# Kernel tuning notes

Measured on AMD Instinct MI355X. Metric: run time of the kernel, lower is better.

## Reference

```python
import jax, jax.numpy as jnp
import numpy as np


def setup_inputs() -> dict:
    key = jax.random.key(0)
    k1, k2, k3 = jax.random.split(key, 3)
    B, C, H, W = 8, 256, 64, 64
    l = jax.random.normal(k1, (B, C, H, W), dtype=jnp.float32)
    # 1x1 conv weights [out=C//2, in=C]; scale 1/sqrt(C) so projected features have ~unit variance
    scale = 1.0 / np.sqrt(C)
    w_theta = jax.random.normal(k2, (C // 2, C), dtype=jnp.float32) * scale
    w_phi = jax.random.normal(k3, (C // 2, C), dtype=jnp.float32) * scale
    return {"l": l, "w_theta": w_theta, "w_phi": w_phi}


def reference(l, w_theta, w_phi):
    # NonLocalOp forward with embed=True, softmax=True
    B, C, H, W = l.shape
    E = w_theta.shape[0]  # C // 2
    HW = H * W
    # 1x1 convs == per-pixel linear maps
    theta = jnp.einsum('bchw,ec->behw', l, w_theta).reshape(B, E, HW)  # [B,E,HW]
    phi = jnp.einsum('bchw,ec->behw', l, w_phi).reshape(B, E, HW)      # [B,E,HW]
    g = l.reshape(B, C, HW)                                            # [B,C,HW]
    # scores: theta^T phi over embed channels, scaled by sqrt(C//2)
    scale = 1.0 / jnp.sqrt(jnp.asarray(C // 2, dtype=l.dtype))
    f = jnp.einsum('beq,bek->bqk', theta, phi) * scale                 # [B,HW,HW]
    f = jax.nn.softmax(f, axis=-1)
    out = jnp.einsum('bqk,bck->bcq', f, g).reshape(B, C, H, W)
    return out
```

## Files before the change

### kernel.cpp

```cpp
#include <hip/hip_runtime.h>
#include <stdint.h>

#define NB 8
#define NC 256
#define NE 128
#define NHW 4096

typedef __bf16 v8bf __attribute__((ext_vector_type(8)));
typedef float v4f __attribute__((ext_vector_type(4)));
typedef float v16f __attribute__((ext_vector_type(16)));

#if __has_builtin(__builtin_amdgcn_exp2f)
#define EXP2F(x) __builtin_amdgcn_exp2f(x)
#else
#define EXP2F(x) exp2f(x)
#endif

__device__ __forceinline__ unsigned short f2bf(float x) {
    union { float f; unsigned int u; } v; v.f = x;
    unsigned int r = v.u + 0x7fffu + ((v.u >> 16) & 1u);
    return (unsigned short)(r >> 16);
}

__global__ __launch_bounds__(256) void cast_w_kernel(const float* __restrict__ wt,
                                                     const float* __restrict__ wp,
                                                     unsigned short* __restrict__ Wbf) {
    int i = blockIdx.x * 256 + threadIdx.x;
    const float QS = 0.08838834764831845f * 1.4426950408889634f;
    float v = (i < 32768) ? wt[i] * QS : wp[i - 32768];
    Wbf[i] = f2bf(v);
}

__global__ __launch_bounds__(256, 2) void proj_kernel(const float* __restrict__ l,
                                                      const unsigned short* __restrict__ Wbf,
                                                      unsigned short* __restrict__ Qbf,
                                                      unsigned short* __restrict__ Kbf,
                                                      unsigned short* __restrict__ Vbf) {
    __shared__ __align__(16) unsigned short A[64][264];
    const int tid = threadIdx.x;
    const int b = blockIdx.x & 7;
    const int qt = (blockIdx.x >> 3) << 6;
    const float* lb = l + ((size_t)b * NC * NHW + qt);

    for (int s = 0; s < 16; ++s) {
        int f = tid + s * 256;
        int c = f >> 4, j = f & 15;
        float4 v = *(const float4*)(lb + (size_t)c * NHW + j * 4);
        ushort4 o4;
        o4.x = f2bf(v.x); o4.y = f2bf(v.y); o4.z = f2bf(v.z); o4.w = f2bf(v.w);
        A[j * 4 + 0][c] = o4.x;
        A[j * 4 + 1][c] = o4.y;
        A[j * 4 + 2][c] = o4.z;
        A[j * 4 + 3][c] = o4.w;
        *(ushort4*)(Vbf + (size_t)b * NC * NHW + (size_t)c * NHW + qt + j * 4) = o4;
    }
    __syncthreads();

    const int w = tid >> 6, L = tid & 63;
    const int l15 = L & 15, q4 = L >> 4;
    const v4f vz = {0.f, 0.f, 0.f, 0.f};
    v4f acc[4][4];
    for (int mt = 0; mt < 4; ++mt)
        for (int nt = 0; nt < 4; ++nt) acc[mt][nt] = vz;

    for (int kf = 0; kf < 8; ++kf) {
        int kc = kf * 32 + q4 * 8;
        v8bf a[4], bb[4];
        for (int mt = 0; mt < 4; ++mt)
            a[mt] = *(const v8bf*)&A[mt * 16 + l15][kc];
        for (int nt = 0; nt < 4; ++nt)
            bb[nt] = *(const v8bf*)(Wbf + (w * 64 + nt * 16 + l15) * 256 + kc);
        for (int mt = 0; mt < 4; ++mt)
            for (int nt = 0; nt < 4; ++nt)
                acc[mt][nt] = __builtin_amdgcn_mfma_f32_16x16x32_bf16(a[mt], bb[nt], acc[mt][nt], 0, 0, 0);
    }

    unsigned short* dst = (w < 2) ? Qbf : Kbf;
    const int ebase = (w & 1) * 64;
    for (int mt = 0; mt < 4; ++mt)
        for (int nt = 0; nt < 4; ++nt)
            for (int r = 0; r < 4; ++r) {
                int q = qt + mt * 16 + q4 * 4 + r;
                int e = ebase + nt * 16 + l15;
                dst[((size_t)b * NHW + q) * NE + e] = f2bf(acc[mt][nt][r]);
            }
}

__global__ __launch_bounds__(256, 2) void attn_kernel(const unsigned short* __restrict__ Qbf,
                                                      const unsigned short* __restrict__ Kbf,
                                                      const unsigned short* __restrict__ Vbf,
                                                      float* __restrict__ out) {
    __shared__ __align__(16) unsigned char smem[57344];
    unsigned short* Ku = (unsigned short*)smem;
    unsigned short* Vu = (unsigned short*)(smem + 16384);
    unsigned short* Pu = (unsigned short*)(smem + 49152);
    float* red = (float*)(smem + 49152);

    const int tid = threadIdx.x;
    const int b = blockIdx.x & 7;
    const int qt64 = (blockIdx.x >> 3) << 6;
    const int w = tid >> 6;
    const int L = tid & 63;
    const int l31 = L & 31, hi = L >> 5;
    const int qh = w >> 1, kh = w & 1;
    const int qhp = w & 1, ctb = (w >> 1) * 4;

    const unsigned short* Kb = Kbf + (size_t)b * NHW * NE;
    const unsigned short* Vb = Vbf + (size_t)b * NC * NHW;

    v8bf aq[8];
    {
        const unsigned short* qrow = Qbf + ((size_t)b * NHW + qt64 + qh * 32 + l31) * NE + hi * 8;
#pragma unroll
        for (int kf = 0; kf < 8; ++kf)
            aq[kf] = *(const v8bf*)(qrow + kf * 16);
    }

    v16f o[4];
#pragma unroll
    for (int ci = 0; ci < 4; ++ci)
#pragma unroll
        for (int r = 0; r < 16; ++r) o[ci][r] = 0.f;
    float lacc[16];
#pragma unroll
    for (int r = 0; r < 16; ++r) lacc[r] = 0.f;

    const int kcol = kh * 32 + l31;
    const int xk = l31 & 15;

    for (int it = 0; it < 64; ++it) {
        const int k0 = it << 6;
        uint4 sk0, sk1, sk2, sk3, sv0, sv1, sv2, sv3, sv4, sv5, sv6, sv7;
        {
            int r0 = tid >> 4, c8 = tid & 15;
            sk0 = *(const uint4*)(Kb + (size_t)(k0 + r0) * NE + c8 * 8);
            sk1 = *(const uint4*)(Kb + (size_t)(k0 + r0 + 16) * NE + c8 * 8);
            sk2 = *(const uint4*)(Kb + (size_t)(k0 + r0 + 32) * NE + c8 * 8);
            sk3 = *(const uint4*)(Kb + (size_t)(k0 + r0 + 48) * NE + c8 * 8);
            int c0 = tid >> 3, u = tid & 7;
            sv0 = *(const uint4*)(Vb + (size_t)(c0 + 0) * NHW + k0 + u * 8);
            sv1 = *(const uint4*)(Vb + (size_t)(c0 + 32) * NHW + k0 + u * 8);
            sv2 = *(const uint4*)(Vb + (size_t)(c0 + 64) * NHW + k0 + u * 8);
            sv3 = *(const uint4*)(Vb + (size_t)(c0 + 96) * NHW + k0 + u * 8);
            sv4 = *(const uint4*)(Vb + (size_t)(c0 + 128) * NHW + k0 + u * 8);
            sv5 = *(const uint4*)(Vb + (size_t)(c0 + 160) * NHW + k0 + u * 8);
            sv6 = *(const uint4*)(Vb + (size_t)(c0 + 192) * NHW + k0 + u * 8);
            sv7 = *(const uint4*)(Vb + (size_t)(c0 + 224) * NHW + k0 + u * 8);
        }
        __syncthreads();
        {
            int r0 = tid >> 4, c8 = tid & 15;
            *(uint4*)&Ku[(r0 + 0) * 128 + ((c8 ^ ((r0 + 0) & 15)) * 8)] = sk0;
            *(uint4*)&Ku[(r0 + 16) * 128 + ((c8 ^ ((r0 + 16) & 15)) * 8)] = sk1;
            *(uint4*)&Ku[(r0 + 32) * 128 + ((c8 ^ ((r0 + 32) & 15)) * 8)] = sk2;
            *(uint4*)&Ku[(r0 + 48) * 128 + ((c8 ^ ((r0 + 48) & 15)) * 8)] = sk3;
            int c0 = tid >> 3, u = tid & 7;
            *(uint4*)&Vu[(c0 + 0) * 64 + ((u ^ ((c0 + 0) & 7)) * 8)] = sv0;
            *(uint4*)&Vu[(c0 + 32) * 64 + ((u ^ ((c0 + 32) & 7)) * 8)] = sv1;
            *(uint4*)&Vu[(c0 + 64) * 64 + ((u ^ ((c0 + 64) & 7)) * 8)] = sv2;
            *(uint4*)&Vu[(c0 + 96) * 64 + ((u ^ ((c0 + 96) & 7)) * 8)] = sv3;
            *(uint4*)&Vu[(c0 + 128) * 64 + ((u ^ ((c0 + 128) & 7)) * 8)] = sv4;
            *(uint4*)&Vu[(c0 + 160) * 64 + ((u ^ ((c0 + 160) & 7)) * 8)] = sv5;
            *(uint4*)&Vu[(c0 + 192) * 64 + ((u ^ ((c0 + 192) & 7)) * 8)] = sv6;
            *(uint4*)&Vu[(c0 + 224) * 64 + ((u ^ ((c0 + 224) & 7)) * 8)] = sv7;
        }
        __syncthreads();

        v16f sa, sb;
#pragma unroll
        for (int r = 0; r < 16; ++r) { sa[r] = 0.f; sb[r] = 0.f; }
        {
            const unsigned short* krow = Ku + kcol * 128;
#pragma unroll
            for (int ef = 0; ef < 4; ++ef) {
                v8bf bk0 = *(const v8bf*)(krow + (((2 * ef + hi) ^ xk) * 8));
                v8bf bk1 = *(const v8bf*)(krow + (((2 * (ef + 4) + hi) ^ xk) * 8));
                sa = __builtin_amdgcn_mfma_f32_32x32x16_bf16(aq[ef], bk0, sa, 0, 0, 0);
                sb = __builtin_amdgcn_mfma_f32_32x32x16_bf16(aq[ef + 4], bk1, sb, 0, 0, 0);
            }
        }

#pragma unroll
        for (int r = 0; r < 16; ++r) {
            float p = EXP2F(sa[r] + sb[r]);
            lacc[r] += p;
            int q = qh * 32 + (r & 3) + 8 * (r >> 2) + 4 * hi;
            Pu[q * 64 + (((kcol >> 3) ^ (q & 7)) * 8) + (kcol & 7)] = f2bf(p);
        }
        __syncthreads();

        v8bf bp[4];
        {
            int qrow = qhp * 32 + l31;
            const unsigned short* prow = Pu + qrow * 64;
            int xq = qrow & 7;
#pragma unroll
            for (int kf = 0; kf < 4; ++kf)
                bp[kf] = *(const v8bf*)(prow + (((kf * 2 + hi) ^ xq) * 8));
        }
#pragma unroll
        for (int kf = 0; kf < 4; ++kf)
#pragma unroll
            for (int ci = 0; ci < 4; ++ci) {
                int c = (ctb + ci) * 32 + l31;
                v8bf av = *(const v8bf*)&Vu[c * 64 + (((kf * 2 + hi) ^ (c & 7)) * 8)];
                o[ci] = __builtin_amdgcn_mfma_f32_32x32x16_bf16(av, bp[kf], o[ci], 0, 0, 0);
            }
    }
    __syncthreads();

#pragma unroll
    for (int r = 0; r < 16; ++r) {
        float v = lacc[r];
        v += __shfl_xor(v, 1);
        v += __shfl_xor(v, 2);
        v += __shfl_xor(v, 4);
        v += __shfl_xor(v, 8);
        v += __shfl_xor(v, 16);
        lacc[r] = v;
    }
    if (l31 == 0) {
#pragma unroll
        for (int r = 0; r < 16; ++r) {
            int q32 = (r & 3) + 8 * (r >> 2) + 4 * hi;
            red[(qh * 2 + kh) * 32 + q32] = lacc[r];
        }
    }
    __syncthreads();
    const float invq = 1.0f / (red[(qhp * 2) * 32 + l31] + red[(qhp * 2 + 1) * 32 + l31]);

    float* ob = out + (size_t)b * NC * NHW + qt64 + qhp * 32 + l31;
#pragma unroll
    for (int ci = 0; ci < 4; ++ci)
#pragma unroll
        for (int r = 0; r < 16; ++r) {
            int c = (ctb + ci) * 32 + (r & 3) + 8 * (r >> 2) + 4 * hi;
            ob[(size_t)c * NHW] = o[ci][r] * invq;
        }
}

extern "C" void kernel_launch(void* const* d_in, const int* in_sizes, int n_in,
                              void* d_out, int out_size, void* d_ws, size_t ws_size,
                              hipStream_t stream) {
    const float* l  = (const float*)d_in[0];
    const float* wt = (const float*)d_in[1];
    const float* wp = (const float*)d_in[2];
    float* out = (float*)d_out;

    char* ws = (char*)d_ws;
    unsigned short* Wbf = (unsigned short*)ws;
    unsigned short* Qbf = (unsigned short*)(ws + 131072);
    unsigned short* Kbf = (unsigned short*)(ws + 131072 + 8388608);
    unsigned short* Vbf = (unsigned short*)(ws + 131072 + 16777216);

    hipLaunchKernelGGL(cast_w_kernel, dim3(256), dim3(256), 0, stream, wt, wp, Wbf);
    hipLaunchKernelGGL(proj_kernel,   dim3(512), dim3(256), 0, stream, l, Wbf, Qbf, Kbf, Vbf);
    hipLaunchKernelGGL(attn_kernel,   dim3(512), dim3(256), 0, stream, Qbf, Kbf, Vbf, out);
}
```

Measured before the change: 237.1 us.

## Load K/V MFMA fragments directly from global, stage Q/K projection stores via LDS

The attention kernel stops staging K and V tiles in shared memory. Each wave now loads its K and V MFMA operand fragments straight from global memory (relying on L2/cache), and the PV product is re-split so each wave owns two channel tiles across both query halves. This shrinks LDS from 56KB to about 8.5KB and drops one barrier per iteration. Separately, the projection kernel stages Q/K results in LDS so they can be written with coalesced 16-byte stores instead of scattered 2-byte ones. The cost is more redundant global/L2 traffic and less latency hiding, since the loads are issued at the top of each iteration with no prefetch.

```diff
diff --git a/kernel.cpp b/kernel.cpp
--- a/kernel.cpp
+++ b/kernel.cpp
@@ -37,6 +37,7 @@
                                                       unsigned short* __restrict__ Kbf,
                                                       unsigned short* __restrict__ Vbf) {
     __shared__ __align__(16) unsigned short A[64][264];
+    __shared__ __align__(16) unsigned short Ost[2][32][136];
     const int tid = threadIdx.x;
     const int b = blockIdx.x & 7;
     const int qt = (blockIdx.x >> 3) << 6;
@@ -75,26 +76,42 @@
                 acc[mt][nt] = __builtin_amdgcn_mfma_f32_16x16x32_bf16(a[mt], bb[nt], acc[mt][nt], 0, 0, 0);
     }
 
-    unsigned short* dst = (w < 2) ? Qbf : Kbf;
+    const int side = w >> 1;
     const int ebase = (w & 1) * 64;
-    for (int mt = 0; mt < 4; ++mt)
-        for (int nt = 0; nt < 4; ++nt)
-            for (int r = 0; r < 4; ++r) {
-                int q = qt + mt * 16 + q4 * 4 + r;
-                int e = ebase + nt * 16 + l15;
-                dst[((size_t)b * NHW + q) * NE + e] = f2bf(acc[mt][nt][r]);
-            }
+#pragma unroll
+    for (int ph = 0; ph < 2; ++ph) {
+        __syncthreads();
+#pragma unroll
+        for (int mh = 0; mh < 2; ++mh) {
+            int mt = ph * 2 + mh;
+#pragma unroll
+            for (int nt = 0; nt < 4; ++nt)
+#pragma unroll
+                for (int r = 0; r < 4; ++r) {
+                    int q32 = mh * 16 + q4 * 4 + r;
+                    Ost[side][q32][ebase + nt * 16 + l15] = f2bf(acc[mt][nt][r]);
+                }
+        }
+        __syncthreads();
+#pragma unroll
+        for (int s = 0; s < 4; ++s) {
+            int idx = tid + s * 256;
+            int sd = idx >> 9, rem = idx & 511;
+            int r32 = rem >> 4, c8 = rem & 15;
+            unsigned short* dst = sd ? Kbf : Qbf;
+            *(uint4*)(dst + ((size_t)b * NHW + qt + ph * 32 + r32) * NE + c8 * 8) =
+                *(const uint4*)&Ost[sd][r32][c8 * 8];
+        }
+    }
 }
 
 __global__ __launch_bounds__(256, 2) void attn_kernel(const unsigned short* __restrict__ Qbf,
                                                       const unsigned short* __restrict__ Kbf,
                                                       const unsigned short* __restrict__ Vbf,
                                                       float* __restrict__ out) {
-    __shared__ __align__(16) unsigned char smem[57344];
-    unsigned short* Ku = (unsigned short*)smem;
-    unsigned short* Vu = (unsigned short*)(smem + 16384);
-    unsigned short* Pu = (unsigned short*)(smem + 49152);
-    float* red = (float*)(smem + 49152);
+    __shared__ __align__(16) unsigned char smem[8704];
+    unsigned short* Pu = (unsigned short*)smem;
+    float* red = (float*)smem;
 
     const int tid = threadIdx.x;
     const int b = blockIdx.x & 7;
@@ -103,7 +120,7 @@
     const int L = tid & 63;
     const int l31 = L & 31, hi = L >> 5;
     const int qh = w >> 1, kh = w & 1;
-    const int qhp = w & 1, ctb = (w >> 1) * 4;
+    const int kcol = kh * 32 + l31;
 
     const unsigned short* Kb = Kbf + (size_t)b * NHW * NE;
     const unsigned short* Vb = Vbf + (size_t)b * NC * NHW;
@@ -112,100 +129,80 @@
     {
         const unsigned short* qrow = Qbf + ((size_t)b * NHW + qt64 + qh * 32 + l31) * NE + hi * 8;
 #pragma unroll
-        for (int kf = 0; kf < 8; ++kf)
-            aq[kf] = *(const v8bf*)(qrow + kf * 16);
-    }
-
-    v16f o[4];
-#pragma unroll
-    for (int ci = 0; ci < 4; ++ci)
-#pragma unroll
-        for (int r = 0; r < 16; ++r) o[ci][r] = 0.f;
+        for (int ef = 0; ef < 8; ++ef)
+            aq[ef] = *(const v8bf*)(qrow + ef * 16);
+    }
+
+    v16f o[2][2];
+#pragma unroll
+    for (int ci = 0; ci < 2; ++ci)
+#pragma unroll
+        for (int qt = 0; qt < 2; ++qt)
+#pragma unroll
+            for (int r = 0; r < 16; ++r) o[ci][qt][r] = 0.f;
     float lacc[16];
 #pragma unroll
     for (int r = 0; r < 16; ++r) lacc[r] = 0.f;
-
-    const int kcol = kh * 32 + l31;
-    const int xk = l31 & 15;
 
     for (int it = 0; it < 64; ++it) {
         const int k0 = it << 6;
-        uint4 sk0, sk1, sk2, sk3, sv0, sv1, sv2, sv3, sv4, sv5, sv6, sv7;
+
+        v8bf bk[8];
         {
-            int r0 = tid >> 4, c8 = tid & 15;
-            sk0 = *(const uint4*)(Kb + (size_t)(k0 + r0) * NE + c8 * 8);
-            sk1 = *(const uint4*)(Kb + (size_t)(k0 + r0 + 16) * NE + c8 * 8);
-            sk2 = *(const uint4*)(Kb + (size_t)(k0 + r0 + 32) * NE + c8 * 8);
-            sk3 = *(const uint4*)(Kb + (size_t)(k0 + r0 + 48) * NE + c8 * 8);
-            int c0 = tid >> 3, u = tid & 7;
-            sv0 = *(const uint4*)(Vb + (size_t)(c0 + 0) * NHW + k0 + u * 8);
-            sv1 = *(const uint4*)(Vb + (size_t)(c0 + 32) * NHW + k0 + u * 8);
-            sv2 = *(const uint4*)(Vb + (size_t)(c0 + 64) * NHW + k0 + u * 8);
-            sv3 = *(const uint4*)(Vb + (size_t)(c0 + 96) * NHW + k0 + u * 8);
-            sv4 = *(const uint4*)(Vb + (size_t)(c0 + 128) * NHW + k0 + u * 8);
-            sv5 = *(const uint4*)(Vb + (size_t)(c0 + 160) * NHW + k0 + u * 8);
-            sv6 = *(const uint4*)(Vb + (size_t)(c0 + 192) * NHW + k0 + u * 8);
-            sv7 = *(const uint4*)(Vb + (size_t)(c0 + 224) * NHW + k0 + u * 8);
-        }
-        __syncthreads();
-        {
-            int r0 = tid >> 4, c8 = tid & 15;
-            *(uint4*)&Ku[(r0 + 0) * 128 + ((c8 ^ ((r0 + 0) & 15)) * 8)] = sk0;
-            *(uint4*)&Ku[(r0 + 16) * 128 + ((c8 ^ ((r0 + 16) & 15)) * 8)] = sk1;
-            *(uint4*)&Ku[(r0 + 32) * 128 + ((c8 ^ ((r0 + 32) & 15)) * 8)] = sk2;
-            *(uint4*)&Ku[(r0 + 48) * 128 + ((c8 ^ ((r0 + 48) & 15)) * 8)] = sk3;
-            int c0 = tid >> 3, u = tid & 7;
-            *(uint4*)&Vu[(c0 + 0) * 64 + ((u ^ ((c0 + 0) & 7)) * 8)] = sv0;
-            *(uint4*)&Vu[(c0 + 32) * 64 + ((u ^ ((c0 + 32) & 7)) * 8)] = sv1;
-            *(uint4*)&Vu[(c0 + 64) * 64 + ((u ^ ((c0 + 64) & 7)) * 8)] = sv2;
-            *(uint4*)&Vu[(c0 + 96) * 64 + ((u ^ ((c0 + 96) & 7)) * 8)] = sv3;
-            *(uint4*)&Vu[(c0 + 128) * 64 + ((u ^ ((c0 + 128) & 7)) * 8)] = sv4;
-            *(uint4*)&Vu[(c0 + 160) * 64 + ((u ^ ((c0 + 160) & 7)) * 8)] = sv5;
-            *(uint4*)&Vu[(c0 + 192) * 64 + ((u ^ ((c0 + 192) & 7)) * 8)] = sv6;
-            *(uint4*)&Vu[(c0 + 224) * 64 + ((u ^ ((c0 + 224) & 7)) * 8)] = sv7;
-        }
-        __syncthreads();
+            const unsigned short* krow = Kb + (size_t)(k0 + kcol) * NE;
+#pragma unroll
+            for (int ef = 0; ef < 8; ++ef)
+                bk[ef] = *(const v8bf*)(krow + (2 * ef + hi) * 8);
+        }
+        v8bf av[2][4];
+#pragma unroll
+        for (int ci = 0; ci < 2; ++ci) {
+            const unsigned short* vrow = Vb + (size_t)((2 * w + ci) * 32 + l31) * NHW + k0;
+#pragma unroll
+            for (int kc = 0; kc < 4; ++kc)
+                av[ci][kc] = *(const v8bf*)(vrow + (2 * kc + hi) * 8);
+        }
 
         v16f sa, sb;
 #pragma unroll
         for (int r = 0; r < 16; ++r) { sa[r] = 0.f; sb[r] = 0.f; }
-        {
-            const unsigned short* krow = Ku + kcol * 128;
-#pragma unroll
-            for (int ef = 0; ef < 4; ++ef) {
-                v8bf bk0 = *(const v8bf*)(krow + (((2 * ef + hi) ^ xk) * 8));
-                v8bf bk1 = *(const v8bf*)(krow + (((2 * (ef + 4) + hi) ^ xk) * 8));
-                sa = __builtin_amdgcn_mfma_f32_32x32x16_bf16(aq[ef], bk0, sa, 0, 0, 0);
-                sb = __builtin_amdgcn_mfma_f32_32x32x16_bf16(aq[ef + 4], bk1, sb, 0, 0, 0);
-            }
-        }
-
+#pragma unroll
+        for (int ef = 0; ef < 4; ++ef) {
+            sa = __builtin_amdgcn_mfma_f32_32x32x16_bf16(aq[ef], bk[ef], sa, 0, 0, 0);
+            sb = __builtin_amdgcn_mfma_f32_32x32x16_bf16(aq[ef + 4], bk[ef + 4], sb, 0, 0, 0);
+        }
+
+        float p[16];
+#pragma unroll
+        for (int r = 0; r < 16; ++r) p[r] = EXP2F(sa[r] + sb[r]);
+#pragma unroll
+        for (int r = 0; r < 16; ++r) lacc[r] += p[r];
+
+        __syncthreads();
 #pragma unroll
         for (int r = 0; r < 16; ++r) {
-            float p = EXP2F(sa[r] + sb[r]);
-            lacc[r] += p;
             int q = qh * 32 + (r & 3) + 8 * (r >> 2) + 4 * hi;
-            Pu[q * 64 + (((kcol >> 3) ^ (q & 7)) * 8) + (kcol & 7)] = f2bf(p);
-        }
-        __syncthreads();
-
-        v8bf bp[4];
-        {
-            int qrow = qhp * 32 + l31;
-            const unsigned short* prow = Pu + qrow * 64;
-            int xq = qrow & 7;
-#pragma unroll
-            for (int kf = 0; kf < 4; ++kf)
-                bp[kf] = *(const v8bf*)(prow + (((kf * 2 + hi) ^ xq) * 8));
-        }
-#pragma unroll
-        for (int kf = 0; kf < 4; ++kf)
-#pragma unroll
-            for (int ci = 0; ci < 4; ++ci) {
-                int c = (ctb + ci) * 32 + l31;
-                v8bf av = *(const v8bf*)&Vu[c * 64 + (((kf * 2 + hi) ^ (c & 7)) * 8)];
-                o[ci] = __builtin_amdgcn_mfma_f32_32x32x16_bf16(av, bp[kf], o[ci], 0, 0, 0);
-            }
+            Pu[q * 64 + (((kcol >> 3) ^ (q & 7)) * 8) + (kcol & 7)] = f2bf(p[r]);
+        }
+        __syncthreads();
+
+        v8bf bp[2][4];
+#pragma unroll
+        for (int qt = 0; qt < 2; ++qt) {
+            int q = qt * 32 + l31;
+            const unsigned short* prow = Pu + q * 64;
+            int xq = q & 7;
+#pragma unroll
+            for (int kc = 0; kc < 4; ++kc)
+                bp[qt][kc] = *(const v8bf*)(prow + (((kc * 2 + hi) ^ xq) * 8));
+        }
+#pragma unroll
+        for (int kc = 0; kc < 4; ++kc)
+#pragma unroll
+            for (int qt = 0; qt < 2; ++qt)
+#pragma unroll
+                for (int ci = 0; ci < 2; ++ci)
+                    o[ci][qt] = __builtin_amdgcn_mfma_f32_32x32x16_bf16(av[ci][kc], bp[qt][kc], o[ci][qt], 0, 0, 0);
     }
     __syncthreads();
 
@@ -227,15 +224,17 @@
         }
     }
     __syncthreads();
-    const float invq = 1.0f / (red[(qhp * 2) * 32 + l31] + red[(qhp * 2 + 1) * 32 + l31]);
-
-    float* ob = out + (size_t)b * NC * NHW + qt64 + qhp * 32 + l31;
-#pragma unroll
-    for (int ci = 0; ci < 4; ++ci)
+    const float inv0 = 1.0f / (red[0 * 32 + l31] + red[1 * 32 + l31]);
+    const float inv1 = 1.0f / (red[2 * 32 + l31] + red[3 * 32 + l31]);
+
+    float* ob = out + (size_t)b * NC * NHW + qt64 + l31;
+#pragma unroll
+    for (int ci = 0; ci < 2; ++ci)
 #pragma unroll
         for (int r = 0; r < 16; ++r) {
-            int c = (ctb + ci) * 32 + (r & 3) + 8 * (r >> 2) + 4 * hi;
-            ob[(size_t)c * NHW] = o[ci][r] * invq;
+            int c = (2 * w + ci) * 32 + (r & 3) + 8 * (r >> 2) + 4 * hi;
+            ob[(size_t)c * NHW + 0] = o[ci][0][r] * inv0;
+            ob[(size_t)c * NHW + 32] = o[ci][1][r] * inv1;
         }
 }
 
```

Result: slower. 326.9 us (+37.9%).
